# Optimization experiments

Hardware: AMD Instinct MI355X
Metric: run time of the kernel (lower is better)

The kernel has to match this reference:

```python
import jax, jax.numpy as jnp
import numpy as np


def setup_inputs() -> dict:
    key = jax.random.key(0)
    k1, k2, k3 = jax.random.split(key, 3)
    shape = (16, 128, 128, 64)  # [B, H, W, C]
    return {
        "query": jax.random.normal(k1, shape, dtype=jnp.float32),
        "keys": jax.random.normal(k2, shape, dtype=jnp.float32),
        "values": jax.random.normal(k3, shape, dtype=jnp.float32),
    }


def reference(query, keys, values):
    # Attention over channel dim C, feature dim = H*W.
    # scores[b, q, k] = sum_{h,w} Q[b,h,w,q] * K[b,h,w,k]
    scores = jnp.einsum("bhwq,bhwk->bqk", query, keys)
    attn = jax.nn.softmax(scores, axis=-1)  # softmax over keys k
    # out[b,h,w,q] = sum_k attn[b,q,k] * V[b,h,w,k]
    out = jnp.einsum("bqk,bhwk->bhwq", attn, values)
    return out
```

## Files before the change

### kernel.cpp

```cpp
#include <hip/hip_runtime.h>


#define S_SPLIT 32
#define CHUNK (16384 / S_SPLIT)
#define TILE_ROWS 32

__global__ __launch_bounds__(256) void scores_kernel(
    const float* __restrict__ Q, const float* __restrict__ K,
    float* __restrict__ partial) {
  const int bs = blockIdx.x;
  const int b = bs / S_SPLIT;
  const int s = bs % S_SPLIT;
  const int tid = threadIdx.x;
  const int w = tid >> 6;
  const int l = tid & 63;
  const int q0 = (l >> 3) * 8;
  const int k0 = (l & 7) * 8;

  __shared__ union {
    struct { float4 q[TILE_ROWS * 16]; float4 k[TILE_ROWS * 16]; } t;
    float red[2][4096];
  } lds;

  float acc[8][8];
#pragma unroll
  for (int i = 0; i < 8; ++i)
#pragma unroll
    for (int j = 0; j < 8; ++j) acc[i][j] = 0.f;

  const float4* Qg = (const float4*)(Q + ((size_t)b * 16384 + (size_t)s * CHUNK) * 64);
  const float4* Kg = (const float4*)(K + ((size_t)b * 16384 + (size_t)s * CHUNK) * 64);

  for (int t = 0; t < CHUNK / TILE_ROWS; ++t) {
    __syncthreads();
    lds.t.q[tid]       = Qg[t * 512 + tid];
    lds.t.q[tid + 256] = Qg[t * 512 + tid + 256];
    lds.t.k[tid]       = Kg[t * 512 + tid];
    lds.t.k[tid + 256] = Kg[t * 512 + tid + 256];
    __syncthreads();

#pragma unroll
    for (int i = 0; i < 8; ++i) {
      const int r = (i << 2) + w;
      float4 qa = lds.t.q[r * 16 + (q0 >> 2)];
      float4 qb = lds.t.q[r * 16 + (q0 >> 2) + 1];
      float4 ka = lds.t.k[r * 16 + (k0 >> 2)];
      float4 kb = lds.t.k[r * 16 + (k0 >> 2) + 1];
      float qv[8] = {qa.x, qa.y, qa.z, qa.w, qb.x, qb.y, qb.z, qb.w};
      float kv[8] = {ka.x, ka.y, ka.z, ka.w, kb.x, kb.y, kb.z, kb.w};
#pragma unroll
      for (int ii = 0; ii < 8; ++ii)
#pragma unroll
        for (int jj = 0; jj < 8; ++jj)
          acc[ii][jj] += qv[ii] * kv[jj];
    }
  }

  __syncthreads();
  if (w >= 2) {
    float4* dst = (float4*)lds.red[w - 2];
#pragma unroll
    for (int i = 0; i < 8; ++i) {
      dst[(q0 + i) * 16 + (k0 >> 2)]     = make_float4(acc[i][0], acc[i][1], acc[i][2], acc[i][3]);
      dst[(q0 + i) * 16 + (k0 >> 2) + 1] = make_float4(acc[i][4], acc[i][5], acc[i][6], acc[i][7]);
    }
  }
  __syncthreads();
  if (w < 2) {
    float4* dst = (float4*)lds.red[w];
#pragma unroll
    for (int i = 0; i < 8; ++i) {
      float4 u = dst[(q0 + i) * 16 + (k0 >> 2)];
      float4 v = dst[(q0 + i) * 16 + (k0 >> 2) + 1];
      dst[(q0 + i) * 16 + (k0 >> 2)]     = make_float4(u.x + acc[i][0], u.y + acc[i][1], u.z + acc[i][2], u.w + acc[i][3]);
      dst[(q0 + i) * 16 + (k0 >> 2) + 1] = make_float4(v.x + acc[i][4], v.y + acc[i][5], v.z + acc[i][6], v.w + acc[i][7]);
    }
  }
  __syncthreads();
  float4* p4 = (float4*)(partial + (size_t)bs * 4096);
  const float4* r0 = (const float4*)lds.red[0];
  const float4* r1 = (const float4*)lds.red[1];
#pragma unroll
  for (int c = 0; c < 4; ++c) {
    float4 x = r0[c * 256 + tid];
    float4 y = r1[c * 256 + tid];
    p4[c * 256 + tid] = make_float4(x.x + y.x, x.y + y.y, x.z + y.z, x.w + y.w);
  }
}

__global__ __launch_bounds__(64) void softmax_kernel(
    const float* __restrict__ partial, float* __restrict__ attn) {
  const int bq = blockIdx.x;
  const int b = bq >> 6;
  const int q = bq & 63;
  const int k = threadIdx.x;

  float v = 0.f;
  for (int s = 0; s < S_SPLIT; ++s)
    v += partial[((size_t)(b * S_SPLIT + s) * 64 + q) * 64 + k];

  float m = v;
#pragma unroll
  for (int off = 32; off > 0; off >>= 1)
    m = fmaxf(m, __shfl_xor(m, off, 64));
  float e = __expf(v - m);
  float sum = e;
#pragma unroll
  for (int off = 32; off > 0; off >>= 1)
    sum += __shfl_xor(sum, off, 64);
  attn[(size_t)bq * 64 + k] = e / sum;
}

__global__ __launch_bounds__(256) void out_kernel(
    const float* __restrict__ V, const float* __restrict__ attn,
    float* __restrict__ out) {
  const int blk = blockIdx.x;
  const int b = blk >> 8;
  const int tile = blk & 255;
  const int tid = threadIdx.x;
  const int w = tid >> 6;
  const int l = tid & 63;

  __shared__ float4 ldsV[64 * 16];

  float a[64];
  const float4* arow = (const float4*)(attn + ((size_t)b * 64 + l) * 64);
#pragma unroll
  for (int j = 0; j < 16; ++j) {
    float4 t = arow[j];
    a[4 * j]     = t.x;
    a[4 * j + 1] = t.y;
    a[4 * j + 2] = t.z;
    a[4 * j + 3] = t.w;
  }

  const float4* Vg = (const float4*)(V + ((size_t)b * 16384 + (size_t)tile * 64) * 64);
#pragma unroll
  for (int c = 0; c < 4; ++c)
    ldsV[c * 256 + tid] = Vg[c * 256 + tid];
  __syncthreads();

  float* outg = out + ((size_t)b * 16384 + (size_t)tile * 64) * 64;
  for (int i = 0; i < 16; ++i) {
    const int r = w * 16 + i;
    float acc = 0.f;
#pragma unroll
    for (int j = 0; j < 16; ++j) {
      float4 v = ldsV[r * 16 + j];
      acc += a[4 * j] * v.x + a[4 * j + 1] * v.y + a[4 * j + 2] * v.z + a[4 * j + 3] * v.w;
    }
    outg[(size_t)r * 64 + l] = acc;
  }
}

extern "C" void kernel_launch(void* const* d_in, const int* in_sizes, int n_in,
                              void* d_out, int out_size, void* d_ws, size_t ws_size,
                              hipStream_t stream) {
  const float* Q = (const float*)d_in[0];
  const float* K = (const float*)d_in[1];
  const float* V = (const float*)d_in[2];
  float* out = (float*)d_out;

  float* partial = (float*)d_ws;
  float* attn = partial + (size_t)16 * S_SPLIT * 4096;

  scores_kernel<<<16 * S_SPLIT, 256, 0, stream>>>(Q, K, partial);
  softmax_kernel<<<16 * 64, 64, 0, stream>>>(partial, attn);
  out_kernel<<<16 * 256, 256, 0, stream>>>(V, attn, out);
}
```

Baseline: 265.9 us.

## Double-buffer scores tiles, vectorize softmax with transposed output, retile out kernel

```diff
diff --git a/kernel.cpp b/kernel.cpp
--- a/kernel.cpp
+++ b/kernel.cpp
@@ -4,6 +4,7 @@
 #define S_SPLIT 32
 #define CHUNK (16384 / S_SPLIT)
 #define TILE_ROWS 32
+#define NT (CHUNK / TILE_ROWS)
 
 __global__ __launch_bounds__(256) void scores_kernel(
     const float* __restrict__ Q, const float* __restrict__ K,
@@ -18,7 +19,7 @@
   const int k0 = (l & 7) * 8;
 
   __shared__ union {
-    struct { float4 q[TILE_ROWS * 16]; float4 k[TILE_ROWS * 16]; } t;
+    struct { float4 q[2][512]; float4 k[2][512]; } t;
     float red[2][4096];
   } lds;
 
@@ -31,21 +32,30 @@
   const float4* Qg = (const float4*)(Q + ((size_t)b * 16384 + (size_t)s * CHUNK) * 64);
   const float4* Kg = (const float4*)(K + ((size_t)b * 16384 + (size_t)s * CHUNK) * 64);
 
-  for (int t = 0; t < CHUNK / TILE_ROWS; ++t) {
+  lds.t.q[0][tid]       = Qg[tid];
+  lds.t.q[0][tid + 256] = Qg[tid + 256];
+  lds.t.k[0][tid]       = Kg[tid];
+  lds.t.k[0][tid + 256] = Kg[tid + 256];
+
+  for (int t = 0; t < NT; ++t) {
     __syncthreads();
-    lds.t.q[tid]       = Qg[t * 512 + tid];
-    lds.t.q[tid + 256] = Qg[t * 512 + tid + 256];
-    lds.t.k[tid]       = Kg[t * 512 + tid];
-    lds.t.k[tid + 256] = Kg[t * 512 + tid + 256];
-    __syncthreads();
+    const int cb = t & 1;
+
+    float4 pq0, pq1, pk0, pk1;
+    if (t + 1 < NT) {
+      pq0 = Qg[(t + 1) * 512 + tid];
+      pq1 = Qg[(t + 1) * 512 + tid + 256];
+      pk0 = Kg[(t + 1) * 512 + tid];
+      pk1 = Kg[(t + 1) * 512 + tid + 256];
+    }
 
 #pragma unroll
     for (int i = 0; i < 8; ++i) {
       const int r = (i << 2) + w;
-      float4 qa = lds.t.q[r * 16 + (q0 >> 2)];
-      float4 qb = lds.t.q[r * 16 + (q0 >> 2) + 1];
-      float4 ka = lds.t.k[r * 16 + (k0 >> 2)];
-      float4 kb = lds.t.k[r * 16 + (k0 >> 2) + 1];
+      float4 qa = lds.t.q[cb][r * 16 + (q0 >> 2)];
+      float4 qb = lds.t.q[cb][r * 16 + (q0 >> 2) + 1];
+      float4 ka = lds.t.k[cb][r * 16 + (k0 >> 2)];
+      float4 kb = lds.t.k[cb][r * 16 + (k0 >> 2) + 1];
       float qv[8] = {qa.x, qa.y, qa.z, qa.w, qb.x, qb.y, qb.z, qb.w};
       float kv[8] = {ka.x, ka.y, ka.z, ka.w, kb.x, kb.y, kb.z, kb.w};
 #pragma unroll
@@ -53,6 +63,14 @@
 #pragma unroll
         for (int jj = 0; jj < 8; ++jj)
           acc[ii][jj] += qv[ii] * kv[jj];
+    }
+
+    if (t + 1 < NT) {
+      const int nb = (t + 1) & 1;
+      lds.t.q[nb][tid]       = pq0;
+      lds.t.q[nb][tid + 256] = pq1;
+      lds.t.k[nb][tid]       = pk0;
+      lds.t.k[nb][tid + 256] = pk1;
     }
   }
 
@@ -89,67 +107,90 @@
 }
 
 __global__ __launch_bounds__(64) void softmax_kernel(
-    const float* __restrict__ partial, float* __restrict__ attn) {
-  const int bq = blockIdx.x;
-  const int b = bq >> 6;
-  const int q = bq & 63;
-  const int k = threadIdx.x;
-
-  float v = 0.f;
-  for (int s = 0; s < S_SPLIT; ++s)
-    v += partial[((size_t)(b * S_SPLIT + s) * 64 + q) * 64 + k];
-
-  float m = v;
-#pragma unroll
-  for (int off = 32; off > 0; off >>= 1)
+    const float* __restrict__ partial, float* __restrict__ attn_t) {
+  const int blk = blockIdx.x;
+  const int b = blk >> 4;
+  const int q0 = (blk & 15) * 4;
+  const int lane = threadIdx.x;
+  const int ql = lane >> 4;
+  const int k4 = lane & 15;
+
+  const float4* P = (const float4*)partial;
+  float4 v = make_float4(0.f, 0.f, 0.f, 0.f);
+  for (int s = 0; s < S_SPLIT; ++s) {
+    float4 t = P[((size_t)(b * S_SPLIT + s) * 64 + q0 + ql) * 16 + k4];
+    v.x += t.x; v.y += t.y; v.z += t.z; v.w += t.w;
+  }
+
+  float m = fmaxf(fmaxf(v.x, v.y), fmaxf(v.z, v.w));
+#pragma unroll
+  for (int off = 8; off > 0; off >>= 1)
     m = fmaxf(m, __shfl_xor(m, off, 64));
-  float e = __expf(v - m);
-  float sum = e;
-#pragma unroll
-  for (int off = 32; off > 0; off >>= 1)
+  float4 e = make_float4(__expf(v.x - m), __expf(v.y - m), __expf(v.z - m), __expf(v.w - m));
+  float sum = e.x + e.y + e.z + e.w;
+#pragma unroll
+  for (int off = 8; off > 0; off >>= 1)
     sum += __shfl_xor(sum, off, 64);
-  attn[(size_t)bq * 64 + k] = e / sum;
+  const float inv = 1.f / sum;
+
+  float* A = attn_t + (size_t)b * 4096;
+  A[(4 * k4 + 0) * 64 + q0 + ql] = e.x * inv;
+  A[(4 * k4 + 1) * 64 + q0 + ql] = e.y * inv;
+  A[(4 * k4 + 2) * 64 + q0 + ql] = e.z * inv;
+  A[(4 * k4 + 3) * 64 + q0 + ql] = e.w * inv;
 }
 
 __global__ __launch_bounds__(256) void out_kernel(
-    const float* __restrict__ V, const float* __restrict__ attn,
+    const float* __restrict__ V, const float* __restrict__ attn_t,
     float* __restrict__ out) {
   const int blk = blockIdx.x;
-  const int b = blk >> 8;
-  const int tile = blk & 255;
+  const int b = blk >> 7;
+  const int tile = blk & 127;
   const int tid = threadIdx.x;
-  const int w = tid >> 6;
-  const int l = tid & 63;
-
-  __shared__ float4 ldsV[64 * 16];
-
-  float a[64];
-  const float4* arow = (const float4*)(attn + ((size_t)b * 64 + l) * 64);
-#pragma unroll
-  for (int j = 0; j < 16; ++j) {
-    float4 t = arow[j];
-    a[4 * j]     = t.x;
-    a[4 * j + 1] = t.y;
-    a[4 * j + 2] = t.z;
-    a[4 * j + 3] = t.w;
-  }
-
-  const float4* Vg = (const float4*)(V + ((size_t)b * 16384 + (size_t)tile * 64) * 64);
-#pragma unroll
-  for (int c = 0; c < 4; ++c)
-    ldsV[c * 256 + tid] = Vg[c * 256 + tid];
-  __syncthreads();
-
-  float* outg = out + ((size_t)b * 16384 + (size_t)tile * 64) * 64;
-  for (int i = 0; i < 16; ++i) {
-    const int r = w * 16 + i;
-    float acc = 0.f;
-#pragma unroll
-    for (int j = 0; j < 16; ++j) {
-      float4 v = ldsV[r * 16 + j];
-      acc += a[4 * j] * v.x + a[4 * j + 1] * v.y + a[4 * j + 2] * v.z + a[4 * j + 3] * v.w;
-    }
-    outg[(size_t)r * 64 + l] = acc;
+  const int g = tid >> 4;
+  const int qg = tid & 15;
+
+  __shared__ float4 Vl[128 * 17];
+  __shared__ float4 Al[64 * 16];
+
+  const float4* Vg = (const float4*)(V + ((size_t)b * 16384 + (size_t)tile * 128) * 64);
+#pragma unroll
+  for (int u = 0; u < 8; ++u) {
+    const int idx = u * 256 + tid;
+    Vl[(idx >> 4) * 17 + (idx & 15)] = Vg[idx];
+  }
+  const float4* Ag = (const float4*)(attn_t + (size_t)b * 4096);
+#pragma unroll
+  for (int u = 0; u < 4; ++u)
+    Al[u * 256 + tid] = Ag[u * 256 + tid];
+  __syncthreads();
+
+  float acc[8][4];
+#pragma unroll
+  for (int i = 0; i < 8; ++i)
+#pragma unroll
+    for (int j = 0; j < 4; ++j) acc[i][j] = 0.f;
+
+  for (int k4 = 0; k4 < 16; ++k4) {
+    const float4 a0 = Al[(4 * k4 + 0) * 16 + qg];
+    const float4 a1 = Al[(4 * k4 + 1) * 16 + qg];
+    const float4 a2 = Al[(4 * k4 + 2) * 16 + qg];
+    const float4 a3 = Al[(4 * k4 + 3) * 16 + qg];
+#pragma unroll
+    for (int i = 0; i < 8; ++i) {
+      const float4 v = Vl[(i * 16 + g) * 17 + k4];
+      acc[i][0] += v.x * a0.x + v.y * a1.x + v.z * a2.x + v.w * a3.x;
+      acc[i][1] += v.x * a0.y + v.y * a1.y + v.z * a2.y + v.w * a3.y;
+      acc[i][2] += v.x * a0.z + v.y * a1.z + v.z * a2.z + v.w * a3.z;
+      acc[i][3] += v.x * a0.w + v.y * a1.w + v.z * a2.w + v.w * a3.w;
+    }
+  }
+
+  float4* og = (float4*)(out + ((size_t)b * 16384 + (size_t)tile * 128) * 64);
+#pragma unroll
+  for (int i = 0; i < 8; ++i) {
+    const int row = i * 16 + g;
+    og[row * 16 + qg] = make_float4(acc[i][0], acc[i][1], acc[i][2], acc[i][3]);
   }
 }
 
@@ -162,9 +203,9 @@
   float* out = (float*)d_out;
 
   float* partial = (float*)d_ws;
-  float* attn = partial + (size_t)16 * S_SPLIT * 4096;
+  float* attn_t = partial + (size_t)16 * S_SPLIT * 4096;
 
   scores_kernel<<<16 * S_SPLIT, 256, 0, stream>>>(Q, K, partial);
-  softmax_kernel<<<16 * 64, 64, 0, stream>>>(partial, attn);
-  out_kernel<<<16 * 256, 256, 0, stream>>>(V, attn, out);
-}
+  softmax_kernel<<<16 * 16, 64, 0, stream>>>(partial, attn_t);
+  out_kernel<<<16 * 128, 256, 0, stream>>>(V, attn_t, out);
+}
```

Result: faster. 227.3 us (-14.5%).
